# Kernel tuning notes

Hardware: AMD Instinct MI355X
Metric: run time of the kernel (lower is better)

Reference implementation:

```python
import jax, jax.numpy as jnp
import numpy as np

B, T, C, H = 8, 2048, 2048, 128  # batch, seq, n_embd, head_size


def setup_inputs() -> dict:
    key = jax.random.key(0)
    kx, kq, kk, kv = jax.random.split(key, 4)
    x = jax.random.normal(kx, (B, T, C), dtype=jnp.float32)
    # Linear(n_embd, head_size, bias=False); stored as [in, out] so x @ W matches x @ weight.T in torch
    Wq = jax.random.normal(kq, (C, H), dtype=jnp.float32) * 0.02
    Wk = jax.random.normal(kk, (C, H), dtype=jnp.float32) * 0.02
    Wv = jax.random.normal(kv, (C, H), dtype=jnp.float32) * 0.02
    return {"x": x, "Wq": Wq, "Wk": Wk, "Wv": Wv}


def reference(x, Wq, Wk, Wv):
    # Single-head scaled dot-product attention (mask=False path of the module)
    q = jnp.einsum("btc,ch->bth", x, Wq)  # [B,T,H]
    k = jnp.einsum("btc,ch->bth", x, Wk)
    v = jnp.einsum("btc,ch->bth", x, Wv)
    scale = k.shape[-1] ** -0.5
    wei = jnp.einsum("bqh,bkh->bqk", q, k) * scale  # [B,T,T]
    wei = jax.nn.softmax(wei, axis=-1)
    out = jnp.einsum("bqk,bkh->bqh", wei, v)  # [B,T,H]
    return out
```

## Files before the change

kernel.cpp:

```cpp
#include <hip/hip_runtime.h>
#include <hip/hip_bf16.h>

typedef __attribute__((ext_vector_type(8))) short short8;
typedef __attribute__((ext_vector_type(4))) float f32x4;

#define MFMA16(a, b, c) __builtin_amdgcn_mfma_f32_16x16x32_bf16((a), (b), (c), 0, 0, 0)

__device__ __forceinline__ unsigned short f2bf(float f) {
    __hip_bfloat16 h = __float2bfloat16(f);
    return __builtin_bit_cast(unsigned short, h);
}

__device__ __forceinline__ short8 cvt8(f32x4 a, f32x4 b) {
    short8 r;
    r[0] = (short)f2bf(a[0]); r[1] = (short)f2bf(a[1]);
    r[2] = (short)f2bf(a[2]); r[3] = (short)f2bf(a[3]);
    r[4] = (short)f2bf(b[0]); r[5] = (short)f2bf(b[1]);
    r[6] = (short)f2bf(b[2]); r[7] = (short)f2bf(b[3]);
    return r;
}

__global__ __launch_bounds__(256) void wt_kernel(const float* __restrict__ Wq,
                                                 const float* __restrict__ Wk,
                                                 const float* __restrict__ Wv,
                                                 unsigned short* __restrict__ Wt) {
    const int j = blockIdx.y;
    const float* W = (j == 0) ? Wq : (j == 1) ? Wk : Wv;
    const int idx = blockIdx.x * 256 + threadIdx.x;
    const int h = idx >> 11;
    const int c = idx & 2047;
    Wt[(size_t)j * (128 * 2048) + idx] = f2bf(W[c * 128 + h]);
}

__global__ __launch_bounds__(256) void qkv_gemm(const float* __restrict__ x,
                                                const unsigned short* __restrict__ Wt,
                                                unsigned short* __restrict__ qkv) {
    constexpr int LDT = 72;
    __shared__ __align__(16) unsigned short As[128 * LDT];
    __shared__ __align__(16) unsigned short Bs[128 * LDT];

    const int tid = threadIdx.x;
    const int l = tid & 63;
    const int w = tid >> 6;
    const int wr = w >> 1, wc = w & 1;
    const int bn = blockIdx.x;
    const int bm = blockIdx.y;
    const int lrow = l & 15, lk = (l >> 4) * 8;

    const float* xA = x + (size_t)bm * 128 * 2048;
    const unsigned short* Wb = Wt + (size_t)bn * (128 * 2048);
    unsigned short* outp = qkv + (size_t)bn * (16384 * 128);

    const f32x4 fzero = {0.f, 0.f, 0.f, 0.f};
    f32x4 acc[4][4];
#pragma unroll
    for (int mt = 0; mt < 4; mt++)
#pragma unroll
        for (int nt = 0; nt < 4; nt++) acc[mt][nt] = fzero;

    for (int kt = 0; kt < 32; kt++) {
        __syncthreads();
#pragma unroll
        for (int i = 0; i < 4; i++) {
            const int c = tid + 256 * i;
            const int m = c >> 3;
            const int k0 = (c & 7) * 8;
            const float* src = xA + (size_t)m * 2048 + kt * 64 + k0;
            f32x4 f0 = *(const f32x4*)(src);
            f32x4 f1 = *(const f32x4*)(src + 4);
            *(short8*)&As[m * LDT + k0] = cvt8(f0, f1);
        }
#pragma unroll
        for (int i = 0; i < 4; i++) {
            const int c = tid + 256 * i;
            const int n = c >> 3;
            const int k0 = (c & 7) * 8;
            short8 bv = *(const short8*)(Wb + (size_t)n * 2048 + kt * 64 + k0);
            *(short8*)&Bs[n * LDT + k0] = bv;
        }
        __syncthreads();
#pragma unroll
        for (int ks = 0; ks < 2; ks++) {
            short8 af[4], bfr[4];
#pragma unroll
            for (int mt = 0; mt < 4; mt++)
                af[mt] = *(const short8*)&As[(wr * 64 + mt * 16 + lrow) * LDT + ks * 32 + lk];
#pragma unroll
            for (int nt = 0; nt < 4; nt++)
                bfr[nt] = *(const short8*)&Bs[(wc * 64 + nt * 16 + lrow) * LDT + ks * 32 + lk];
#pragma unroll
            for (int mt = 0; mt < 4; mt++)
#pragma unroll
                for (int nt = 0; nt < 4; nt++)
                    acc[mt][nt] = MFMA16(af[mt], bfr[nt], acc[mt][nt]);
        }
    }

    const float scale = (bn == 0) ? 0.08838834764831845f : 1.0f;
#pragma unroll
    for (int mt = 0; mt < 4; mt++)
#pragma unroll
        for (int nt = 0; nt < 4; nt++)
#pragma unroll
            for (int r = 0; r < 4; r++) {
                const int row = bm * 128 + wr * 64 + mt * 16 + (l >> 4) * 4 + r;
                const int col = wc * 64 + nt * 16 + lrow;
                outp[(size_t)row * 128 + col] = f2bf(acc[mt][nt][r] * scale);
            }
}

__global__ __launch_bounds__(256) void attn_kernel(const unsigned short* __restrict__ q,
                                                   const unsigned short* __restrict__ k,
                                                   const unsigned short* __restrict__ v,
                                                   float* __restrict__ out) {
    constexpr int KS = 136;
    constexpr int VS = 88;
    constexpr int PS = 88;
    __shared__ __align__(16) unsigned short Ks[64 * KS];
    __shared__ __align__(16) unsigned short Vt[128 * VS];
    __shared__ __align__(16) unsigned short Psh[64 * PS];

    const int tid = threadIdx.x;
    const int l = tid & 63;
    const int w = tid >> 6;
    const int qt = blockIdx.x;
    const int b = blockIdx.y;
    const int lrow = l & 15, g = l >> 4, lk = g * 8;

    const size_t qbase = ((size_t)b * 2048 + qt * 64 + w * 16 + lrow) * 128;
    short8 qf[4];
#pragma unroll
    for (int ks = 0; ks < 4; ks++) qf[ks] = *(const short8*)(q + qbase + ks * 32 + lk);

    const f32x4 fzero = {0.f, 0.f, 0.f, 0.f};
    float m_r[4], l_r[4];
    f32x4 oacc[8];
#pragma unroll
    for (int r = 0; r < 4; r++) { m_r[r] = -1e30f; l_r[r] = 0.f; }
#pragma unroll
    for (int d = 0; d < 8; d++) oacc[d] = fzero;

    const int skey = tid & 63;
    const int sd = (tid >> 6) * 8;

    for (int kv = 0; kv < 32; kv++) {
        __syncthreads();
        const size_t kvbase = ((size_t)b * 2048 + kv * 64 + skey) * 128;
#pragma unroll
        for (int jj = 0; jj < 4; jj++) {
            const int d0 = sd + jj * 32;
            short8 kvv = *(const short8*)(k + kvbase + d0);
            *(short8*)&Ks[skey * KS + d0] = kvv;
        }
#pragma unroll
        for (int jj = 0; jj < 4; jj++) {
            const int d0 = sd + jj * 32;
            short8 vv = *(const short8*)(v + kvbase + d0);
#pragma unroll
            for (int e = 0; e < 8; e++)
                Vt[(d0 + e) * VS + skey] = (unsigned short)vv[e];
        }
        __syncthreads();

        f32x4 s[4];
#pragma unroll
        for (int nt = 0; nt < 4; nt++) s[nt] = fzero;
#pragma unroll
        for (int ks = 0; ks < 4; ks++)
#pragma unroll
            for (int nt = 0; nt < 4; nt++) {
                short8 kf = *(const short8*)&Ks[(nt * 16 + lrow) * KS + ks * 32 + lk];
                s[nt] = MFMA16(qf[ks], kf, s[nt]);
            }

        float sf[4];
#pragma unroll
        for (int r = 0; r < 4; r++) {
            float tmax = fmaxf(fmaxf(s[0][r], s[1][r]), fmaxf(s[2][r], s[3][r]));
#pragma unroll
            for (int mk = 8; mk >= 1; mk >>= 1) tmax = fmaxf(tmax, __shfl_xor(tmax, mk));
            const float mnew = fmaxf(m_r[r], tmax);
            sf[r] = __expf(m_r[r] - mnew);
            m_r[r] = mnew;
            float psum = 0.f;
#pragma unroll
            for (int nt = 0; nt < 4; nt++) {
                const float p = __expf(s[nt][r] - mnew);
                s[nt][r] = p;
                psum += p;
            }
#pragma unroll
            for (int mk = 8; mk >= 1; mk >>= 1) psum += __shfl_xor(psum, mk);
            l_r[r] = l_r[r] * sf[r] + psum;
        }
#pragma unroll
        for (int d = 0; d < 8; d++)
#pragma unroll
            for (int r = 0; r < 4; r++) oacc[d][r] *= sf[r];

#pragma unroll
        for (int nt = 0; nt < 4; nt++)
#pragma unroll
            for (int r = 0; r < 4; r++)
                Psh[(w * 16 + g * 4 + r) * PS + nt * 16 + lrow] = f2bf(s[nt][r]);
        __syncthreads();

#pragma unroll
        for (int ks2 = 0; ks2 < 2; ks2++) {
            short8 pa = *(const short8*)&Psh[(w * 16 + lrow) * PS + ks2 * 32 + lk];
#pragma unroll
            for (int dt = 0; dt < 8; dt++) {
                short8 vbf = *(const short8*)&Vt[(dt * 16 + lrow) * VS + ks2 * 32 + lk];
                oacc[dt] = MFMA16(pa, vbf, oacc[dt]);
            }
        }
    }

#pragma unroll
    for (int r = 0; r < 4; r++) {
        const float inv = 1.0f / l_r[r];
        const size_t rowbase = ((size_t)b * 2048 + qt * 64 + w * 16 + g * 4 + r) * 128;
#pragma unroll
        for (int dt = 0; dt < 8; dt++)
            out[rowbase + dt * 16 + lrow] = oacc[dt][r] * inv;
    }
}

extern "C" void kernel_launch(void* const* d_in, const int* in_sizes, int n_in,
                              void* d_out, int out_size, void* d_ws, size_t ws_size,
                              hipStream_t stream) {
    const float* x  = (const float*)d_in[0];
    const float* Wq = (const float*)d_in[1];
    const float* Wk = (const float*)d_in[2];
    const float* Wv = (const float*)d_in[3];
    float* out = (float*)d_out;

    unsigned short* ws = (unsigned short*)d_ws;
    unsigned short* qb = ws;
    unsigned short* kb = qb + (size_t)16384 * 128;
    unsigned short* vb = kb + (size_t)16384 * 128;
    unsigned short* Wt = vb + (size_t)16384 * 128;

    hipLaunchKernelGGL(wt_kernel, dim3(1024, 3), dim3(256), 0, stream, Wq, Wk, Wv, Wt);
    hipLaunchKernelGGL(qkv_gemm, dim3(3, 128), dim3(256), 0, stream, x, Wt, qb);
    hipLaunchKernelGGL(attn_kernel, dim3(32, 8), dim3(256), 0, stream, qb, kb, vb, out);
}
```

Measured before the change: 324.2 us.

## Split attention KV range three ways with merge kernel; tile weight transpose

The attention kernel's KV loop is split into three chunks across a new grid dimension. This triples block count from 256 to 768 so more of the GPU's compute units are occupied. Partial unnormalized outputs and running max/sum go to workspace, and a new merge kernel combines them with log-sum-exp rescaling. The weight transpose kernel now uses a shared-memory tiled transpose with vectorized loads and stores. The change adds an extra kernel launch and extra fp32 global traffic for the partials, and falls back to the unsplit path if the workspace is too small.

```diff
diff --git a/kernel.cpp b/kernel.cpp
--- a/kernel.cpp
+++ b/kernel.cpp
@@ -24,12 +24,33 @@
                                                  const float* __restrict__ Wk,
                                                  const float* __restrict__ Wv,
                                                  unsigned short* __restrict__ Wt) {
-    const int j = blockIdx.y;
+    __shared__ float T[64][65];
+    const int j = blockIdx.z;
     const float* W = (j == 0) ? Wq : (j == 1) ? Wk : Wv;
-    const int idx = blockIdx.x * 256 + threadIdx.x;
-    const int h = idx >> 11;
-    const int c = idx & 2047;
-    Wt[(size_t)j * (128 * 2048) + idx] = f2bf(W[c * 128 + h]);
+    const int c0 = blockIdx.x * 64;
+    const int h0 = blockIdx.y * 64;
+    const int tid = threadIdx.x;
+
+#pragma unroll
+    for (int i = 0; i < 4; i++) {
+        const int cc = tid + 256 * i;
+        const int r = cc >> 4;
+        const int q4 = (cc & 15) * 4;
+        f32x4 vv = *(const f32x4*)(W + (size_t)(c0 + r) * 128 + h0 + q4);
+        T[r][q4 + 0] = vv[0]; T[r][q4 + 1] = vv[1];
+        T[r][q4 + 2] = vv[2]; T[r][q4 + 3] = vv[3];
+    }
+    __syncthreads();
+#pragma unroll
+    for (int i = 0; i < 2; i++) {
+        const int oc = tid + 256 * i;
+        const int hr = oc >> 3;
+        const int c8 = (oc & 7) * 8;
+        short8 r;
+#pragma unroll
+        for (int e = 0; e < 8; e++) r[e] = (short)f2bf(T[c8 + e][hr]);
+        *(short8*)(Wt + (size_t)j * (128 * 2048) + (size_t)(h0 + hr) * 2048 + c0 + c8) = r;
+    }
 }
 
 __global__ __launch_bounds__(256) void qkv_gemm(const float* __restrict__ x,
@@ -109,10 +130,12 @@
             }
 }
 
-__global__ __launch_bounds__(256) void attn_kernel(const unsigned short* __restrict__ q,
-                                                   const unsigned short* __restrict__ k,
-                                                   const unsigned short* __restrict__ v,
-                                                   float* __restrict__ out) {
+template <bool SPLIT>
+__global__ __launch_bounds__(256) void attn_kernel_t(const unsigned short* __restrict__ q,
+                                                     const unsigned short* __restrict__ k,
+                                                     const unsigned short* __restrict__ v,
+                                                     float* __restrict__ Oout,
+                                                     float* __restrict__ Ml) {
     constexpr int KS = 136;
     constexpr int VS = 88;
     constexpr int PS = 88;
@@ -125,6 +148,9 @@
     const int w = tid >> 6;
     const int qt = blockIdx.x;
     const int b = blockIdx.y;
+    const int s = SPLIT ? blockIdx.z : 0;
+    const int kv_beg = SPLIT ? s * 11 : 0;
+    const int kv_end = SPLIT ? ((s == 2) ? 32 : kv_beg + 11) : 32;
     const int lrow = l & 15, g = l >> 4, lk = g * 8;
 
     const size_t qbase = ((size_t)b * 2048 + qt * 64 + w * 16 + lrow) * 128;
@@ -143,7 +169,7 @@
     const int skey = tid & 63;
     const int sd = (tid >> 6) * 8;
 
-    for (int kv = 0; kv < 32; kv++) {
+    for (int kv = kv_beg; kv < kv_end; kv++) {
         __syncthreads();
         const size_t kvbase = ((size_t)b * 2048 + kv * 64 + skey) * 128;
 #pragma unroll
@@ -162,21 +188,21 @@
         }
         __syncthreads();
 
-        f32x4 s[4];
-#pragma unroll
-        for (int nt = 0; nt < 4; nt++) s[nt] = fzero;
+        f32x4 sv[4];
+#pragma unroll
+        for (int nt = 0; nt < 4; nt++) sv[nt] = fzero;
 #pragma unroll
         for (int ks = 0; ks < 4; ks++)
 #pragma unroll
             for (int nt = 0; nt < 4; nt++) {
                 short8 kf = *(const short8*)&Ks[(nt * 16 + lrow) * KS + ks * 32 + lk];
-                s[nt] = MFMA16(qf[ks], kf, s[nt]);
+                sv[nt] = MFMA16(qf[ks], kf, sv[nt]);
             }
 
         float sf[4];
 #pragma unroll
         for (int r = 0; r < 4; r++) {
-            float tmax = fmaxf(fmaxf(s[0][r], s[1][r]), fmaxf(s[2][r], s[3][r]));
+            float tmax = fmaxf(fmaxf(sv[0][r], sv[1][r]), fmaxf(sv[2][r], sv[3][r]));
 #pragma unroll
             for (int mk = 8; mk >= 1; mk >>= 1) tmax = fmaxf(tmax, __shfl_xor(tmax, mk));
             const float mnew = fmaxf(m_r[r], tmax);
@@ -185,8 +211,8 @@
             float psum = 0.f;
 #pragma unroll
             for (int nt = 0; nt < 4; nt++) {
-                const float p = __expf(s[nt][r] - mnew);
-                s[nt][r] = p;
+                const float p = __expf(sv[nt][r] - mnew);
+                sv[nt][r] = p;
                 psum += p;
             }
 #pragma unroll
@@ -202,7 +228,7 @@
         for (int nt = 0; nt < 4; nt++)
 #pragma unroll
             for (int r = 0; r < 4; r++)
-                Psh[(w * 16 + g * 4 + r) * PS + nt * 16 + lrow] = f2bf(s[nt][r]);
+                Psh[(w * 16 + g * 4 + r) * PS + nt * 16 + lrow] = f2bf(sv[nt][r]);
         __syncthreads();
 
 #pragma unroll
@@ -218,12 +244,41 @@
 
 #pragma unroll
     for (int r = 0; r < 4; r++) {
-        const float inv = 1.0f / l_r[r];
-        const size_t rowbase = ((size_t)b * 2048 + qt * 64 + w * 16 + g * 4 + r) * 128;
-#pragma unroll
-        for (int dt = 0; dt < 8; dt++)
-            out[rowbase + dt * 16 + lrow] = oacc[dt][r] * inv;
-    }
+        const int rowi = b * 2048 + qt * 64 + w * 16 + g * 4 + r;
+        if (SPLIT) {
+            const size_t obase = ((size_t)s * 16384 + rowi) * 128;
+#pragma unroll
+            for (int dt = 0; dt < 8; dt++)
+                Oout[obase + dt * 16 + lrow] = oacc[dt][r];
+            if (lrow == 0) {
+                const size_t mb = ((size_t)s * 16384 + rowi) * 2;
+                Ml[mb] = m_r[r];
+                Ml[mb + 1] = l_r[r];
+            }
+        } else {
+            const float inv = 1.0f / l_r[r];
+#pragma unroll
+            for (int dt = 0; dt < 8; dt++)
+                Oout[(size_t)rowi * 128 + dt * 16 + lrow] = oacc[dt][r] * inv;
+        }
+    }
+}
+
+__global__ __launch_bounds__(256) void attn_merge(const float* __restrict__ Oacc,
+                                                  const float* __restrict__ Ml,
+                                                  float* __restrict__ out) {
+    const int row = blockIdx.x * 2 + (threadIdx.x >> 7);
+    const int c = threadIdx.x & 127;
+    const float m0 = Ml[(size_t)(0 * 16384 + row) * 2], l0 = Ml[(size_t)(0 * 16384 + row) * 2 + 1];
+    const float m1 = Ml[(size_t)(1 * 16384 + row) * 2], l1 = Ml[(size_t)(1 * 16384 + row) * 2 + 1];
+    const float m2 = Ml[(size_t)(2 * 16384 + row) * 2], l2 = Ml[(size_t)(2 * 16384 + row) * 2 + 1];
+    const float M = fmaxf(m0, fmaxf(m1, m2));
+    const float w0 = __expf(m0 - M), w1 = __expf(m1 - M), w2 = __expf(m2 - M);
+    const float D = w0 * l0 + w1 * l1 + w2 * l2;
+    const float o = w0 * Oacc[(size_t)(0 * 16384 + row) * 128 + c] +
+                    w1 * Oacc[(size_t)(1 * 16384 + row) * 128 + c] +
+                    w2 * Oacc[(size_t)(2 * 16384 + row) * 128 + c];
+    out[(size_t)row * 128 + c] = o / D;
 }
 
 extern "C" void kernel_launch(void* const* d_in, const int* in_sizes, int n_in,
@@ -240,8 +295,18 @@
     unsigned short* kb = qb + (size_t)16384 * 128;
     unsigned short* vb = kb + (size_t)16384 * 128;
     unsigned short* Wt = vb + (size_t)16384 * 128;
-
-    hipLaunchKernelGGL(wt_kernel, dim3(1024, 3), dim3(256), 0, stream, Wq, Wk, Wv, Wt);
+    float* Oacc = (float*)(Wt + (size_t)3 * 128 * 2048);
+    float* Ml = Oacc + (size_t)3 * 16384 * 128;
+    const size_t ws_need = (size_t)((char*)(Ml + (size_t)3 * 16384 * 2) - (char*)d_ws);
+
+    hipLaunchKernelGGL(wt_kernel, dim3(32, 2, 3), dim3(256), 0, stream, Wq, Wk, Wv, Wt);
     hipLaunchKernelGGL(qkv_gemm, dim3(3, 128), dim3(256), 0, stream, x, Wt, qb);
-    hipLaunchKernelGGL(attn_kernel, dim3(32, 8), dim3(256), 0, stream, qb, kb, vb, out);
-}
+    if (ws_size >= ws_need) {
+        hipLaunchKernelGGL((attn_kernel_t<true>), dim3(32, 8, 3), dim3(256), 0, stream,
+                           qb, kb, vb, Oacc, Ml);
+        hipLaunchKernelGGL(attn_merge, dim3(8192), dim3(256), 0, stream, Oacc, Ml, out);
+    } else {
+        hipLaunchKernelGGL((attn_kernel_t<false>), dim3(32, 8), dim3(256), 0, stream,
+                           qb, kb, vb, out, (float*)nullptr);
+    }
+}
```

New measurement: 295.9 us. 8.7% less time.
